# Kernel tuning notes

Hardware: AMD Instinct MI355X
Metric: run time of the kernel (lower is better)

## Reference

```python
import jax, jax.numpy as jnp
import numpy as np

NEG_FILL = -100.0  # matches torch new_full(-100.0) init for scatter-amax


def reference(x, part_labels, parts_num=16):
    # x: (n, c, s, h, w) float; part_labels: (n, s, h, w) int in [0, parts_num)
    n, c, s, h, w = x.shape
    hw = h * w
    ns = n * s
    # (n s) c (h w)
    feat = jnp.transpose(x, (0, 2, 1, 3, 4)).reshape(ns, c, hw)
    labels = part_labels.reshape(ns, hw).astype(jnp.int32)

    b3 = jnp.arange(ns)[:, None, None]          # (ns,1,1)
    ch = jnp.arange(c)[None, :, None]            # (1,c,1)
    lbl3 = labels[:, None, :]                    # (ns,1,hw) -> broadcasts to (ns,c,hw)

    pooled_sum = jnp.zeros((ns, c, parts_num), x.dtype).at[b3, ch, lbl3].add(feat)
    b2 = jnp.arange(ns)[:, None]
    pooled_count = jnp.zeros((ns, parts_num), x.dtype).at[b2, labels].add(1.0)  # (ns,P)
    pooled_max = jnp.full((ns, c, parts_num), NEG_FILL, x.dtype).at[b3, ch, lbl3].max(feat)

    count = pooled_count[:, None, :]             # (ns,1,P)
    pooled_mean = pooled_sum / jnp.maximum(count, 1.0)
    pooled_max = jnp.where(count > 0, pooled_max, 0.0)
    pooled = pooled_mean + pooled_max            # (ns,c,P)
    # (n s) c p -> n c s p
    return jnp.transpose(pooled.reshape(n, s, c, parts_num), (0, 2, 1, 3))


def setup_inputs() -> dict:
    key = jax.random.key(0)
    k1, k2 = jax.random.split(key)
    n, c, s, h, w = 16, 256, 32, 16, 11
    parts_num = 16
    x = jax.random.normal(k1, (n, c, s, h, w), dtype=jnp.float32)
    part_labels = jax.random.randint(k2, (n, s, h, w), 0, parts_num, dtype=jnp.int64)
    return {"x": x, "part_labels": part_labels, "parts_num": parts_num}
```

## Files before the change

### kernel.cpp

```cpp
#include <hip/hip_runtime.h>


constexpr int C   = 256;
constexpr int S   = 32;
constexpr int HW  = 176;
constexpr int P   = 16;
constexpr int ROW = S * HW;
constexpr float NEG_FILL = -100.0f;

constexpr int BSTRIDE  = 64;
constexpr int META_U16 = P * BSTRIDE + P;
constexpr int GC    = 16;
constexpr int PITCH = 180;

__global__ __launch_bounds__(192) void prep_kernel(const int* __restrict__ labels,
                                                   unsigned short* __restrict__ ws)
{
    __shared__ int fill[P];
    __shared__ unsigned short perm[P * BSTRIDE];
    const int tid = threadIdx.x, ns = blockIdx.x;
    if (tid < P) fill[tid] = 0;
    __syncthreads();
    if (tid < HW) {
        int l = labels[ns * HW + tid];
        int r = atomicAdd(&fill[l], 1);
        if (r < BSTRIDE) perm[(l << 6) + r] = (unsigned short)tid;
    }
    __syncthreads();
    unsigned*       wp = (unsigned*)(ws + (size_t)ns * META_U16);
    const unsigned* sp = (const unsigned*)perm;
    for (int i = tid; i < (P * BSTRIDE) / 2; i += 192) wp[i] = sp[i];
    if (tid < P)
        ws[(size_t)ns * META_U16 + P * BSTRIDE + tid] =
            (unsigned short)min(fill[tid], BSTRIDE);
}

template <bool USE_WS>
__global__ __launch_bounds__(256) void hpp_main(const float* __restrict__ x,
                                                const int*   __restrict__ labels,
                                                const unsigned short* __restrict__ ws,
                                                float* __restrict__ out)
{
    __shared__ float          tile[GC * PITCH];
    __shared__ unsigned short meta[META_U16];
    __shared__ int            fill[P];

    const int tid = threadIdx.x;
    const int blk = blockIdx.x;
    const int ns  = blk >> 4, cg = blk & 15;
    const int n   = ns >> 5,  s  = ns & 31;

    const float* xb = x + (size_t)(n * C + cg * GC) * ROW + s * HW;
    const int f0 = tid, f1 = tid + 256, f2 = tid + 512;
    const int r0 = f0 / 44, j0 = f0 - r0 * 44;
    const int r1 = f1 / 44, j1 = f1 - r1 * 44;
    const int r2 = f2 / 44, j2 = f2 - r2 * 44;
    float4 v0 = *(const float4*)(xb + (size_t)r0 * ROW + j0 * 4);
    float4 v1 = *(const float4*)(xb + (size_t)r1 * ROW + j1 * 4);
    float4 v2;
    const bool has2 = (f2 < GC * 44);
    if (has2) v2 = *(const float4*)(xb + (size_t)r2 * ROW + j2 * 4);

    if (USE_WS) {
        const unsigned* w = (const unsigned*)(ws + (size_t)ns * META_U16);
        unsigned*       m = (unsigned*)meta;
        m[tid]       = w[tid];
        m[tid + 256] = w[tid + 256];
        if (tid < 8) m[tid + 512] = w[tid + 512];
    } else {
        if (tid < P) fill[tid] = 0;
        __syncthreads();
        if (tid < HW) {
            int l = labels[ns * HW + tid];
            int r = atomicAdd(&fill[l], 1);
            if (r < BSTRIDE) meta[(l << 6) + r] = (unsigned short)tid;
        }
        __syncthreads();
        if (tid < P) meta[P * BSTRIDE + tid] = (unsigned short)min(fill[tid], BSTRIDE);
    }

    *(float4*)&tile[r0 * PITCH + j0 * 4] = v0;
    *(float4*)&tile[r1 * PITCH + j1 * 4] = v1;
    if (has2) *(float4*)&tile[r2 * PITCH + j2 * 4] = v2;
    __syncthreads();

    const int c = tid >> 4, p = tid & 15;
    const int k = meta[P * BSTRIDE + p];
    const unsigned short* pp = &meta[p << 6];
    const float*          tc = &tile[c * PITCH];
    float sum = 0.f, mx = NEG_FILL;
    int j = 0;
    for (; j + 1 < k; j += 2) {
        unsigned u = *(const unsigned*)&pp[j];
        float a = tc[u & 0xFFFFu];
        float b = tc[u >> 16];
        sum += a; mx = fmaxf(mx, a);
        sum += b; mx = fmaxf(mx, b);
    }
    if (j < k) { float a = tc[pp[j]]; sum += a; mx = fmaxf(mx, a); }

    float res = (k > 0) ? sum / (float)k + mx : 0.f;
    out[((size_t)(n * C + cg * GC + c) * S + s) * P + p] = res;
}

extern "C" void kernel_launch(void* const* d_in, const int* in_sizes, int n_in,
                              void* d_out, int out_size, void* d_ws, size_t ws_size,
                              hipStream_t stream) {
    const float* x      = (const float*)d_in[0];
    const int*   labels = (const int*)d_in[1];
    float*       out    = (float*)d_out;

    const int ns_total = in_sizes[1] / HW;
    const int nblk     = ns_total * (C / GC);
    const size_t need  = (size_t)ns_total * META_U16 * sizeof(unsigned short);

    if (ws_size >= need) {
        prep_kernel<<<ns_total, 192, 0, stream>>>(labels, (unsigned short*)d_ws);
        hpp_main<true><<<nblk, 256, 0, stream>>>(x, labels, (const unsigned short*)d_ws, out);
    } else {
        hpp_main<false><<<nblk, 256, 0, stream>>>(x, labels, nullptr, out);
    }
}
```

Before: 140.9 us.

## Fuse label bucketing into main kernel and use byte-index buckets with split accumulators

Drops the separate prep kernel and workspace path, so each block builds its own per-part index buckets from the labels. Bucket indices shrink to bytes, letting four indices come from one 32-bit load, and two independent sum/max accumulators shorten the dependency chain. The thread mapping changes to p-major with c in the low bits, the tile pitch changes to 178 with float2 stores, and the labels load is issued before the x loads. This removes a kernel launch and a global workspace round trip, but every block redoes the label bucketing work.

```diff
diff --git a/kernel.cpp b/kernel.cpp
--- a/kernel.cpp
+++ b/kernel.cpp
@@ -6,49 +6,28 @@
 constexpr int HW  = 176;
 constexpr int P   = 16;
 constexpr int ROW = S * HW;
+constexpr int GC  = 16;
+constexpr int PITCH = 178;
+constexpr int BCAP  = 64;
 constexpr float NEG_FILL = -100.0f;
 
-constexpr int BSTRIDE  = 64;
-constexpr int META_U16 = P * BSTRIDE + P;
-constexpr int GC    = 16;
-constexpr int PITCH = 180;
-
-__global__ __launch_bounds__(192) void prep_kernel(const int* __restrict__ labels,
-                                                   unsigned short* __restrict__ ws)
+__global__ __launch_bounds__(256) void hpp_kernel(
+    const float* __restrict__ x,
+    const int*   __restrict__ labels,
+    float*       __restrict__ out)
 {
-    __shared__ int fill[P];
-    __shared__ unsigned short perm[P * BSTRIDE];
-    const int tid = threadIdx.x, ns = blockIdx.x;
-    if (tid < P) fill[tid] = 0;
-    __syncthreads();
-    if (tid < HW) {
-        int l = labels[ns * HW + tid];
-        int r = atomicAdd(&fill[l], 1);
-        if (r < BSTRIDE) perm[(l << 6) + r] = (unsigned short)tid;
-    }
-    __syncthreads();
-    unsigned*       wp = (unsigned*)(ws + (size_t)ns * META_U16);
-    const unsigned* sp = (const unsigned*)perm;
-    for (int i = tid; i < (P * BSTRIDE) / 2; i += 192) wp[i] = sp[i];
-    if (tid < P)
-        ws[(size_t)ns * META_U16 + P * BSTRIDE + tid] =
-            (unsigned short)min(fill[tid], BSTRIDE);
-}
-
-template <bool USE_WS>
-__global__ __launch_bounds__(256) void hpp_main(const float* __restrict__ x,
-                                                const int*   __restrict__ labels,
-                                                const unsigned short* __restrict__ ws,
-                                                float* __restrict__ out)
-{
-    __shared__ float          tile[GC * PITCH];
-    __shared__ unsigned short meta[META_U16];
-    __shared__ int            fill[P];
+    __shared__ float         tile[GC * PITCH];
+    __shared__ unsigned char perm[P * BCAP];
+    __shared__ int           cnt[P];
 
     const int tid = threadIdx.x;
     const int blk = blockIdx.x;
     const int ns  = blk >> 4, cg = blk & 15;
     const int n   = ns >> 5,  s  = ns & 31;
+
+    const int* ln = labels + (size_t)ns * HW;
+    int lab = 0;
+    if (tid < HW) lab = ln[tid];
 
     const float* xb = x + (size_t)(n * C + cg * GC) * ROW + s * HW;
     const int f0 = tid, f1 = tid + 256, f2 = tid + 512;
@@ -57,49 +36,60 @@
     const int r2 = f2 / 44, j2 = f2 - r2 * 44;
     float4 v0 = *(const float4*)(xb + (size_t)r0 * ROW + j0 * 4);
     float4 v1 = *(const float4*)(xb + (size_t)r1 * ROW + j1 * 4);
-    float4 v2;
+    float4 v2 = make_float4(0.f, 0.f, 0.f, 0.f);
     const bool has2 = (f2 < GC * 44);
     if (has2) v2 = *(const float4*)(xb + (size_t)r2 * ROW + j2 * 4);
 
-    if (USE_WS) {
-        const unsigned* w = (const unsigned*)(ws + (size_t)ns * META_U16);
-        unsigned*       m = (unsigned*)meta;
-        m[tid]       = w[tid];
-        m[tid + 256] = w[tid + 256];
-        if (tid < 8) m[tid + 512] = w[tid + 512];
-    } else {
-        if (tid < P) fill[tid] = 0;
-        __syncthreads();
-        if (tid < HW) {
-            int l = labels[ns * HW + tid];
-            int r = atomicAdd(&fill[l], 1);
-            if (r < BSTRIDE) meta[(l << 6) + r] = (unsigned short)tid;
+    ((unsigned*)perm)[tid] = 0u;
+    if (tid < P) cnt[tid] = 0;
+    __syncthreads();
+    if (tid < HW) {
+        int r = atomicAdd(&cnt[lab], 1);
+        if (r < BCAP) perm[(lab << 6) + r] = (unsigned char)tid;
+    }
+    __syncthreads();
+
+    {
+        float2* t0 = (float2*)&tile[r0 * PITCH + j0 * 4];
+        t0[0] = make_float2(v0.x, v0.y); t0[1] = make_float2(v0.z, v0.w);
+        float2* t1 = (float2*)&tile[r1 * PITCH + j1 * 4];
+        t1[0] = make_float2(v1.x, v1.y); t1[1] = make_float2(v1.z, v1.w);
+        if (has2) {
+            float2* t2 = (float2*)&tile[r2 * PITCH + j2 * 4];
+            t2[0] = make_float2(v2.x, v2.y); t2[1] = make_float2(v2.z, v2.w);
         }
-        __syncthreads();
-        if (tid < P) meta[P * BSTRIDE + tid] = (unsigned short)min(fill[tid], BSTRIDE);
+    }
+    __syncthreads();
+
+    const int p = tid >> 4, c = tid & 15;
+    const int k = min(cnt[p], BCAP);
+    const unsigned char* pp = &perm[p << 6];
+    const float*         tc = &tile[c * PITCH];
+
+    float s0 = 0.f, s1 = 0.f, m0 = NEG_FILL, m1 = NEG_FILL;
+    const int kf = k & ~3;
+    for (int j = 0; j < kf; j += 4) {
+        unsigned u = *(const unsigned*)&pp[j];
+        float a0 = tc[u & 0xFF];
+        float a1 = tc[(u >> 8) & 0xFF];
+        float a2 = tc[(u >> 16) & 0xFF];
+        float a3 = tc[u >> 24];
+        s0 += a0; m0 = fmaxf(m0, a0);
+        s1 += a1; m1 = fmaxf(m1, a1);
+        s0 += a2; m0 = fmaxf(m0, a2);
+        s1 += a3; m1 = fmaxf(m1, a3);
+    }
+    if (kf < k) {
+        unsigned u = *(const unsigned*)&pp[kf];
+        float a0 = tc[u & 0xFF];
+        float a1 = tc[(u >> 8) & 0xFF];
+        float a2 = tc[(u >> 16) & 0xFF];
+        s0 += a0; m0 = fmaxf(m0, a0);
+        if (kf + 1 < k) { s1 += a1; m1 = fmaxf(m1, a1); }
+        if (kf + 2 < k) { s0 += a2; m0 = fmaxf(m0, a2); }
     }
 
-    *(float4*)&tile[r0 * PITCH + j0 * 4] = v0;
-    *(float4*)&tile[r1 * PITCH + j1 * 4] = v1;
-    if (has2) *(float4*)&tile[r2 * PITCH + j2 * 4] = v2;
-    __syncthreads();
-
-    const int c = tid >> 4, p = tid & 15;
-    const int k = meta[P * BSTRIDE + p];
-    const unsigned short* pp = &meta[p << 6];
-    const float*          tc = &tile[c * PITCH];
-    float sum = 0.f, mx = NEG_FILL;
-    int j = 0;
-    for (; j + 1 < k; j += 2) {
-        unsigned u = *(const unsigned*)&pp[j];
-        float a = tc[u & 0xFFFFu];
-        float b = tc[u >> 16];
-        sum += a; mx = fmaxf(mx, a);
-        sum += b; mx = fmaxf(mx, b);
-    }
-    if (j < k) { float a = tc[pp[j]]; sum += a; mx = fmaxf(mx, a); }
-
-    float res = (k > 0) ? sum / (float)k + mx : 0.f;
+    float res = (k > 0) ? (s0 + s1) / (float)k + fmaxf(m0, m1) : 0.f;
     out[((size_t)(n * C + cg * GC + c) * S + s) * P + p] = res;
 }
 
@@ -112,12 +102,5 @@
 
     const int ns_total = in_sizes[1] / HW;
     const int nblk     = ns_total * (C / GC);
-    const size_t need  = (size_t)ns_total * META_U16 * sizeof(unsigned short);
-
-    if (ws_size >= need) {
-        prep_kernel<<<ns_total, 192, 0, stream>>>(labels, (unsigned short*)d_ws);
-        hpp_main<true><<<nblk, 256, 0, stream>>>(x, labels, (const unsigned short*)d_ws, out);
-    } else {
-        hpp_main<false><<<nblk, 256, 0, stream>>>(x, labels, nullptr, out);
-    }
+    hpp_kernel<<<nblk, 256, 0, stream>>>(x, labels, out);
 }
```

Measured after the change: 134.6 us. -4.5%, faster.
